# Performance work log

Hardware: AMD Instinct MI355X
Metric: run time of the kernel (lower is better)

## Reference

```python
import jax, jax.numpy as jnp
import numpy as np

NUM_ROUTES = 8 * 17 * 17  # 2312
NUM_CAPS = 10
OUT_CH = 16
IN_CH = 8


def squash(x, axis):
    sn = jnp.sum(x * x, axis=axis, keepdims=True)
    return sn * x / ((1.0 + sn) * jnp.sqrt(sn))


def setup_inputs() -> dict:
    key = jax.random.key(0)
    ks = jax.random.split(key, 11)
    B = 128
    data = jax.random.normal(ks[0], (B, 3, 49, 49), dtype=jnp.float32)
    conv_w = jax.random.normal(ks[1], (32, 3, 9, 9), dtype=jnp.float32) * 0.06
    conv_b = jax.random.normal(ks[2], (32,), dtype=jnp.float32) * 0.01
    # 8 primary-capsule convs, each 32->8, stacked: [8, 8, 32, 9, 9]
    prim_w = jax.random.normal(ks[3], (8, 8, 32, 9, 9), dtype=jnp.float32) * 0.02
    prim_b = jax.random.normal(ks[4], (8, 8), dtype=jnp.float32) * 0.01
    # DigitCaps W: torch used plain randn, shape [num_routes, num_caps, out, in]
    W_digit = jax.random.normal(ks[5], (NUM_ROUTES, NUM_CAPS, OUT_CH, IN_CH), dtype=jnp.float32)
    head_w1 = jax.random.normal(ks[6], (NUM_CAPS, 16, 100), dtype=jnp.float32) * 0.25
    head_b1 = jax.random.normal(ks[7], (NUM_CAPS, 100), dtype=jnp.float32) * 0.01
    head_w2 = jax.random.normal(ks[8], (NUM_CAPS, 100, 1), dtype=jnp.float32) * 0.1
    head_b2 = jax.random.normal(ks[9], (NUM_CAPS, 1), dtype=jnp.float32) * 0.01
    return {"data": data, "conv_w": conv_w, "conv_b": conv_b,
            "prim_w": prim_w, "prim_b": prim_b, "W_digit": W_digit,
            "head_w1": head_w1, "head_b1": head_b1,
            "head_w2": head_w2, "head_b2": head_b2}


def _forward(data, conv_w, conv_b, prim_w, prim_b, W_digit,
             head_w1, head_b1, head_w2, head_b2):
    dn = ("NCHW", "OIHW", "NCHW")
    # Conv stem: [B,3,49,49] -> [B,32,41,41], ReLU
    x = jax.lax.conv_general_dilated(data, conv_w, (1, 1), "VALID",
                                     dimension_numbers=dn)
    x = jax.nn.relu(x + conv_b[None, :, None, None])
    B = x.shape[0]
    # PrimaryCaps: 8 convs 32->8, k9 s2 -> [B,64,17,17] via merged weight
    pw = prim_w.reshape(64, 32, 9, 9)
    pb = prim_b.reshape(64)
    u = jax.lax.conv_general_dilated(x, pw, (2, 2), "VALID",
                                     dimension_numbers=dn)
    u = u + pb[None, :, None, None]
    u = u.reshape(B, 8, NUM_ROUTES)          # [B, 8 capsules, 2312]
    u = squash(u, axis=2)
    # DigitCaps: x_t [B, routes, in=8]; u_hat [B, routes, caps, out=16]
    x_t = u.transpose(0, 2, 1)
    u_hat = jnp.einsum("rcoi,bri->brco", W_digit, x_t)
    b_ij = jnp.zeros((NUM_ROUTES, NUM_CAPS), dtype=u_hat.dtype)
    v = None
    for it in range(3):
        c = jax.nn.softmax(b_ij, axis=1)                       # over capsules
        s = jnp.einsum("rc,brco->bco", c, u_hat)               # [B,caps,out]
        v = squash(s, axis=-1)                                 # [B,caps,16]
        if it < 2:
            a = jnp.einsum("brco,bco->brc", u_hat, v).mean(axis=0)
            b_ij = b_ij + a
    output = v[:, :, :, None]                                  # [B,10,16,1]
    # 10 tiny heads: head k applied to capsule k
    h = jnp.tanh(jnp.einsum("bci,cih->bch", v, head_w1) + head_b1[None])
    logits = jnp.einsum("bch,cho->bco", h, head_w2) + head_b2[None]
    cls = jax.nn.sigmoid(logits)                                # [B,10,1]
    return (output,) + tuple(cls[:, k] for k in range(NUM_CAPS))


def reference(data, conv_w, conv_b, prim_w, prim_b, W_digit,
              head_w1, head_b1, head_w2, head_b2):
    return _forward(data, conv_w, conv_b, prim_w, prim_b, W_digit,
                    head_w1, head_b1, head_w2, head_b2)
```

## Files before the change

kernel.cpp:

```cpp
#include <hip/hip_runtime.h>
#include <math.h>

#define BATCH 128
#define NR 2312
#define RC 34
#define NCH 68
#define NC 10
#define K1 352

typedef short short8 __attribute__((ext_vector_type(8)));
typedef float f32x4 __attribute__((ext_vector_type(4)));
typedef unsigned long long u64;

#define OFF_XH    0
#define OFF_XTB   3442688
#define OFF_SC    4630528
#define OFF_BIJ   4631552
#define OFF_SP    4654672
#define OFF_V     6047312
#define OFF_WB    6067792
#define OFF_VT    6150736
#define OFF_W1    6171216

__device__ __forceinline__ unsigned short f2bf(float f) {
    unsigned int u = __float_as_uint(f);
    u = (u + 0x7FFFu + ((u >> 16) & 1u)) >> 16;
    return (unsigned short)u;
}
__device__ __forceinline__ float bf2f(unsigned short h) {
    return __uint_as_float(((unsigned int)h) << 16);
}

__global__ void k_prep(const float* __restrict__ cw, const float* __restrict__ pw,
                       unsigned short* __restrict__ W1, unsigned short* __restrict__ Wb,
                       float* __restrict__ bij, float* __restrict__ scale) {
    int idx = blockIdx.x * 256 + threadIdx.x;
    if (idx < 165888) {
        int ci = idx & 31, co = (idx >> 5) & 15, cog = (idx >> 9) & 3, tap = idx >> 11;
        Wb[idx] = f2bf(pw[((cog * 16 + co) * 32 + ci) * 81 + tap]);
        return;
    }
    idx -= 165888;
    if (idx < 23120) { bij[idx] = 0.f; return; }
    idx -= 23120;
    if (idx < 1024) { scale[idx] = 0.f; return; }
    idx -= 1024;
    if (idx < 32 * K1) {
        int co = idx / K1, k = idx - co * K1;
        int g = k / 12, kw = k - g * 12;
        float v = (kw < 9 && g < 27) ? cw[((co * 3 + g / 9) * 9 + (g % 9)) * 9 + kw] : 0.f;
        W1[idx] = f2bf(v);
    }
}

__global__ __launch_bounds__(512) void k_conv1m(const float* __restrict__ data,
                                                const unsigned short* __restrict__ W1,
                                                const float* __restrict__ cb,
                                                unsigned short* __restrict__ xh) {
    int b = blockIdx.x / 27, g64 = blockIdx.x % 27;
    int p0 = g64 * 64;
    int t = threadIdx.x, lane = t & 63, wv = t >> 6;
    int quad = lane >> 4, mloc = lane & 15;
    int msub = wv & 3, chh = wv >> 2;
    __shared__ __align__(16) unsigned short As[88 * 64 * 4];
    u64* ab = (u64*)As;
    for (int k = 81 * 64 + t; k < 88 * 64; k += 512) ab[k] = 0ull;
#pragma unroll 1
    for (int it = 0; it < 4; it++) {
        int g = wv + it * 8;
        if (g < 27) {
            int m = lane;
            int p = p0 + m; if (p > 1680) p = 1680;
            int h = p / 41, w = p - h * 41;
            int ci = g / 9, kh = g - ci * 9;
            const float* src = &data[((b * 3 + ci) * 49 + (h + kh)) * 49 + w];
            unsigned short pk[12];
#pragma unroll
            for (int kw = 0; kw < 9; kw++) pk[kw] = f2bf(src[kw]);
            pk[9] = 0; pk[10] = 0; pk[11] = 0;
            const u64* s = (const u64*)pk;
            ab[(3 * g + 0) * 64 + m] = s[0];
            ab[(3 * g + 1) * 64 + m] = s[1];
            ab[(3 * g + 2) * 64 + m] = s[2];
        }
    }
    __syncthreads();
    f32x4 acc = {0.f, 0.f, 0.f, 0.f};
    const unsigned short* wp = &W1[(size_t)(chh * 16 + mloc) * K1 + quad * 8];
    int mrow = msub * 16 + mloc;
#pragma unroll 1
    for (int kc = 0; kc < 11; kc++) {
        int c = kc * 8 + quad * 2;
        union { short8 v; u64 q[2]; } af;
        af.q[0] = ab[c * 64 + mrow];
        af.q[1] = ab[(c + 1) * 64 + mrow];
        short8 bfr = *(const short8*)(wp + kc * 32);
        acc = __builtin_amdgcn_mfma_f32_16x16x32_bf16(af.v, bfr, acc, 0, 0, 0);
    }
    __syncthreads();
    unsigned short* tile = As;
    float bias = cb[chh * 16 + mloc];
#pragma unroll
    for (int r = 0; r < 4; r++) {
        int m = msub * 16 + quad * 4 + r;
        float v0 = acc[r] + bias; v0 = v0 > 0.f ? v0 : 0.f;
        tile[m * 40 + chh * 16 + mloc] = f2bf(v0);
    }
    __syncthreads();
    if (t < 256) {
        int m = t >> 2, part = t & 3;
        int p = p0 + m;
        if (p < 1681)
            *(int4*)&xh[((size_t)(b * 1681 + p)) * 32 + part * 8] =
                *(const int4*)&tile[m * 40 + part * 8];
    }
}

__global__ __launch_bounds__(512) void k_conv2(const unsigned short* __restrict__ xh,
                                               const unsigned short* __restrict__ Wb,
                                               const float* __restrict__ pb,
                                               unsigned short* __restrict__ xTb,
                                               float* __restrict__ scale) {
    const int pstart[5] = {0, 73, 145, 217, 289};
    int b = blockIdx.x >> 2, g = blockIdx.x & 3;
    int p0 = pstart[g], np = pstart[g + 1] - p0;
    int r0 = 2 * (p0 / 17);
    int t = threadIdx.x, lane = t & 63, wv = t >> 6;
    int quad = lane >> 4, mloc = lane & 15;
    int cg = wv & 3, th = wv >> 2;
    __shared__ __align__(16) char lds[50184];
    __shared__ float pbs[64];
    unsigned short* As = (unsigned short*)lds;
    if (t < 64) pbs[t] = pb[t];
    const unsigned short* xb = xh + (size_t)b * 53792;
    for (int k = t; k < 17 * 164; k += 512) {
        int rl = k / 164, rem = k - rl * 164;
        int col = rem >> 2, ci8 = rem & 3;
        int e = (col & 1) ? 21 + (col >> 1) : (col >> 1);
        const u64* src = (const u64*)&xb[((r0 + rl) * 41 + col) * 32 + ci8 * 8];
        u64* dst = (u64*)&As[(rl * 41 + e) * 36 + ci8 * 8];
        dst[0] = src[0];
        dst[1] = src[1];
    }
    __syncthreads();
    int abase[5];
#pragma unroll
    for (int mt = 0; mt < 5; mt++) {
        int p = p0 + mt * 16 + mloc;
        if (p > 288) p = 288;
        abase[mt] = ((2 * (p / 17) - r0) * 41 + (p % 17)) * 36 + quad * 8;
    }
    const unsigned short* wbase = Wb + ((size_t)cg * 16 + mloc) * 32 + quad * 8;
    f32x4 acc[5];
#pragma unroll
    for (int mt = 0; mt < 5; mt++)
#pragma unroll
        for (int r = 0; r < 4; r++) acc[mt][r] = 0.f;
    int kh0 = th ? 5 : 0, kh1 = th ? 9 : 5;
#pragma unroll 1
    for (int kh = kh0; kh < kh1; kh++) {
        const unsigned short* wrow = wbase + (size_t)kh * 9 * 2048;
#pragma unroll
        for (int kw = 0; kw < 9; kw++) {
            short8 bf = *(const short8*)(wrow + (size_t)kw * 2048);
            int c0 = (kw & 1) ? 21 + (kw >> 1) : (kw >> 1);
            int off = (kh * 41 + c0) * 36;
#pragma unroll
            for (int mt = 0; mt < 5; mt++) {
                union { short8 v; u64 q[2]; } a;
                a.q[0] = *(const u64*)&As[abase[mt] + off];
                a.q[1] = *(const u64*)&As[abase[mt] + off + 4];
                acc[mt] = __builtin_amdgcn_mfma_f32_16x16x32_bf16(a.v, bf, acc[mt], 0, 0, 0);
            }
        }
    }
    __syncthreads();
    float* tile = (float*)lds;
    if (th == 0) {
#pragma unroll
        for (int mt = 0; mt < 5; mt++)
#pragma unroll
            for (int r = 0; r < 4; r++)
                tile[(cg * 16 + mloc) * 81 + mt * 16 + quad * 4 + r] = acc[mt][r];
    }
    __syncthreads();
    if (th == 1) {
#pragma unroll
        for (int mt = 0; mt < 5; mt++)
#pragma unroll
            for (int r = 0; r < 4; r++)
                tile[(cg * 16 + mloc) * 81 + mt * 16 + quad * 4 + r] += acc[mt][r];
    }
    __syncthreads();
    float ssq[8] = {0.f, 0.f, 0.f, 0.f, 0.f, 0.f, 0.f, 0.f};
#pragma unroll 1
    for (int idx = t; idx < 8 * np; idx += 512) {
        int pp = idx >> 3, j = idx & 7;
        unsigned short pk[8];
#pragma unroll
        for (int i = 0; i < 8; i++) {
            float val = tile[(i * 8 + j) * 81 + pp] + pbs[i * 8 + j];
            pk[i] = f2bf(val);
            ssq[i] += val * val;
        }
        *(int4*)&xTb[((size_t)(j * 289 + p0 + pp) * 128 + b) * 8] = *(const int4*)pk;
    }
#pragma unroll
    for (int i = 0; i < 8; i++) {
        float s = ssq[i];
#pragma unroll
        for (int d = 1; d < 64; d <<= 1) s += __shfl_xor(s, d);
        if (lane == 0) atomicAdd(&scale[b * 8 + i], s);
    }
}

__global__ __launch_bounds__(256) void k_xt(unsigned short* __restrict__ xTb,
                                            const float* __restrict__ scale) {
    __shared__ float fs[1024];
    int t = threadIdx.x;
    for (int k = t; k < 1024; k += 256) {
        float sn = scale[k];
        fs[k] = sn / ((1.f + sn) * sqrtf(sn));
    }
    __syncthreads();
    int idx = blockIdx.x * 256 + t;
    int b = idx & 127;
    unsigned short* p = &xTb[(size_t)idx * 8];
    union { int4 v; unsigned short u[8]; } d;
    d.v = *(const int4*)p;
#pragma unroll
    for (int i = 0; i < 8; i++) d.u[i] = f2bf(bf2f(d.u[i]) * fs[b * 8 + i]);
    *(int4*)p = d.v;
}

__global__ __launch_bounds__(256) void k_s(const unsigned short* __restrict__ xTb,
                                           const float* __restrict__ W,
                                           const float* __restrict__ bij,
                                           float* __restrict__ spart) {
    int chunk = blockIdx.x / NC, c = blockIdx.x % NC;
    int r0 = chunk * RC;
    __shared__ __align__(16) unsigned short As[16 * 296];
    __shared__ float cs[RC];
    int t = threadIdx.x;
    { int o = t >> 4, kk = t & 15; As[o * 296 + 272 + kk] = 0; }
    if (t < RC) {
        int r = r0 + t;
        float x[NC], m = -1e30f;
#pragma unroll
        for (int k = 0; k < NC; k++) { x[k] = bij[r * NC + k]; m = fmaxf(m, x[k]); }
        float s = 0.f;
#pragma unroll
        for (int k = 0; k < NC; k++) { x[k] = expf(x[k] - m); s += x[k]; }
        cs[t] = x[c] / s;
    }
    __syncthreads();
    for (int k = t; k < RC * 16; k += 256) {
        int rr = k >> 4, o = k & 15;
        const float* wsrc = &W[(size_t)(r0 + rr) * 1280 + c * 128 + o * 8];
        float cr = cs[rr];
        unsigned short pk[8];
#pragma unroll
        for (int i = 0; i < 8; i++) pk[i] = f2bf(wsrc[i] * cr);
        *(int4*)&As[o * 296 + rr * 8] = *(const int4*)pk;
    }
    __syncthreads();
    int lane = t & 63, wv = t >> 6;
    int quad = lane >> 4, mloc = lane & 15;
    int n0 = wv * 32;
    f32x4 acc0 = {0.f, 0.f, 0.f, 0.f}, acc1 = {0.f, 0.f, 0.f, 0.f};
    const unsigned short* ap = &As[mloc * 296 + quad * 8];
#pragma unroll
    for (int kc = 0; kc < 9; kc++) {
        short8 af = *(const short8*)(ap + kc * 32);
        const unsigned short* bb = &xTb[(size_t)(r0 + kc * 4 + quad) * 1024];
        short8 b0 = *(const short8*)(bb + (n0 + mloc) * 8);
        short8 b1 = *(const short8*)(bb + (n0 + 16 + mloc) * 8);
        acc0 = __builtin_amdgcn_mfma_f32_16x16x32_bf16(af, b0, acc0, 0, 0, 0);
        acc1 = __builtin_amdgcn_mfma_f32_16x16x32_bf16(af, b1, acc1, 0, 0, 0);
    }
    float* sp = &spart[(size_t)(chunk * NC + c) * 2048];
    *(f32x4*)&sp[(n0 + mloc) * 16 + quad * 4] = acc0;
    *(f32x4*)&sp[(n0 + 16 + mloc) * 16 + quad * 4] = acc1;
}

__global__ __launch_bounds__(256) void k_v(const float* __restrict__ spart,
                    float* __restrict__ v, float* __restrict__ vT,
                    float* __restrict__ out,
                    const float* __restrict__ w1, const float* __restrict__ b1,
                    const float* __restrict__ w2, const float* __restrict__ b2,
                    int do_head) {
    int b = blockIdx.x / NC, c = blockIdx.x % NC;
    int t = threadIdx.x;
    int cl = t >> 4, o = t & 15;
    float s = 0.f;
#pragma unroll 1
    for (int ch = cl; ch < NCH; ch += 16)
        s += spart[((size_t)(ch * NC + c) * 128 + b) * 16 + o];
    s += __shfl_xor(s, 16);
    s += __shfl_xor(s, 32);
    __shared__ float red[4][16];
    __shared__ float hred[2];
    if ((t & 63) < 16) red[t >> 6][t & 15] = s;
    __syncthreads();
    if (t < 16) {
        float sum = red[0][t] + red[1][t] + red[2][t] + red[3][t];
        float sq = sum * sum;
#pragma unroll
        for (int d = 1; d < 16; d <<= 1) sq += __shfl_xor(sq, d);
        float vv = sum * sq / ((1.f + sq) * sqrtf(sq));
        int idx = (b * NC + c) * 16 + t;
        v[idx] = vv;
        out[idx] = vv;
        vT[(c * 16 + t) * 128 + b] = vv;
        red[0][t] = vv;
    }
    if (do_head) {
        __syncthreads();
        float partial = 0.f;
        if (t < 100) {
            float hs = b1[c * 100 + t];
#pragma unroll
            for (int i = 0; i < 16; i++) hs = fmaf(red[0][i], w1[(c * 16 + i) * 100 + t], hs);
            partial = tanhf(hs) * w2[c * 100 + t];
        }
#pragma unroll
        for (int d = 1; d < 64; d <<= 1) partial += __shfl_xor(partial, d);
        if ((t & 63) == 0 && t < 128) hred[t >> 6] = partial;
        __syncthreads();
        if (t == 0)
            out[20480 + c * 128 + b] = 1.f / (1.f + expf(-(hred[0] + hred[1] + b2[c])));
    }
}

__global__ __launch_bounds__(256) void k_a(const unsigned short* __restrict__ xTb,
                                           const float* __restrict__ W,
                                           const float* __restrict__ vT,
                                           float* __restrict__ bij) {
    int wv = threadIdx.x >> 6, lane = threadIdx.x & 63;
    int wid = __builtin_amdgcn_readfirstlane(blockIdx.x * 4 + wv);
    int r = wid / NC, c = wid - r * NC;
    const unsigned short* xr = &xTb[(size_t)r * 1024];
    union { short8 v; unsigned short u[8]; } s0, s1;
    s0.v = *(const short8*)(xr + lane * 8);
    s1.v = *(const short8*)(xr + (lane + 64) * 8);
    float x0[8], x1[8];
#pragma unroll
    for (int i = 0; i < 8; i++) { x0[i] = bf2f(s0.u[i]); x1[i] = bf2f(s1.u[i]); }
    const float* wr = &W[(size_t)r * 1280 + c * 128];
    const float* vc = &vT[c * 2048];
    float acc = 0.f;
#pragma unroll
    for (int o = 0; o < 16; o++) {
        float w[8];
#pragma unroll
        for (int i = 0; i < 8; i++) w[i] = wr[o * 8 + i];
        float u0 = 0.f, u1 = 0.f;
#pragma unroll
        for (int i = 0; i < 8; i++) { u0 = fmaf(w[i], x0[i], u0); u1 = fmaf(w[i], x1[i], u1); }
        acc = fmaf(vc[o * 128 + lane], u0, acc);
        acc = fmaf(vc[o * 128 + lane + 64], u1, acc);
    }
#pragma unroll
    for (int d = 1; d < 64; d <<= 1) acc += __shfl_xor(acc, d);
    if (lane == 0) bij[wid] += acc * 0.0078125f;
}

extern "C" void kernel_launch(void* const* d_in, const int* in_sizes, int n_in,
                              void* d_out, int out_size, void* d_ws, size_t ws_size,
                              hipStream_t stream) {
    const float* data   = (const float*)d_in[0];
    const float* conv_w = (const float*)d_in[1];
    const float* conv_b = (const float*)d_in[2];
    const float* prim_w = (const float*)d_in[3];
    const float* prim_b = (const float*)d_in[4];
    const float* Wd     = (const float*)d_in[5];
    const float* hw1    = (const float*)d_in[6];
    const float* hb1    = (const float*)d_in[7];
    const float* hw2    = (const float*)d_in[8];
    const float* hb2    = (const float*)d_in[9];
    float* ws = (float*)d_ws;
    unsigned short* xh  = (unsigned short*)(ws + OFF_XH);
    unsigned short* xTb = (unsigned short*)(ws + OFF_XTB);
    float* scale = ws + OFF_SC;
    float* bij   = ws + OFF_BIJ;
    float* spart = ws + OFF_SP;
    float* v     = ws + OFF_V;
    unsigned short* Wb  = (unsigned short*)(ws + OFF_WB);
    float* vT    = ws + OFF_VT;
    unsigned short* W1  = (unsigned short*)(ws + OFF_W1);
    float* out = (float*)d_out;

    k_prep<<<787, 256, 0, stream>>>(conv_w, prim_w, W1, Wb, bij, scale);
    k_conv1m<<<128 * 27, 512, 0, stream>>>(data, W1, conv_b, xh);
    k_conv2<<<128 * 4, 512, 0, stream>>>(xh, Wb, prim_b, xTb, scale);
    k_xt<<<1156, 256, 0, stream>>>(xTb, scale);
    for (int it = 0; it < 3; it++) {
        k_s<<<NCH * NC, 256, 0, stream>>>(xTb, Wd, bij, spart);
        k_v<<<128 * NC, 256, 0, stream>>>(spart, v, vT, out, hw1, hb1, hw2, hb2,
                                          it == 2 ? 1 : 0);
        if (it < 2) k_a<<<5780, 256, 0, stream>>>(xTb, Wd, vT, bij);
    }
}
```

Baseline: 234.0 us.

## Repartition primary-caps conv into 64-position tiles with M-split warps instead of K-split

The conv2 kernel now splits each image into 5 blocks of 64 output positions instead of 4 uneven groups. The two warp halves now take different M tiles (32 positions each, 2 accumulators) over the full 9x9 kernel, rather than splitting kh and summing partial results. This removes the two-pass reduction through shared memory and the extra MFMA tiles that were wasted on padding. It raises the grid to 640 blocks so more CUs get work, at the cost of more redundant halo loads of input rows per block.

```diff
diff --git a/kernel.cpp b/kernel.cpp
--- a/kernel.cpp
+++ b/kernel.cpp
@@ -121,19 +121,20 @@
                                                const float* __restrict__ pb,
                                                unsigned short* __restrict__ xTb,
                                                float* __restrict__ scale) {
-    const int pstart[5] = {0, 73, 145, 217, 289};
-    int b = blockIdx.x >> 2, g = blockIdx.x & 3;
-    int p0 = pstart[g], np = pstart[g + 1] - p0;
-    int r0 = 2 * (p0 / 17);
+    int b = blockIdx.x / 5, g = blockIdx.x % 5;
     int t = threadIdx.x, lane = t & 63, wv = t >> 6;
     int quad = lane >> 4, mloc = lane & 15;
-    int cg = wv & 3, th = wv >> 2;
+    int cg = wv & 3, half = wv >> 2;
     __shared__ __align__(16) char lds[50184];
     __shared__ float pbs[64];
     unsigned short* As = (unsigned short*)lds;
     if (t < 64) pbs[t] = pb[t];
     const unsigned short* xb = xh + (size_t)b * 53792;
-    for (int k = t; k < 17 * 164; k += 512) {
+    int p_hi = g * 64 + 63; if (p_hi > 288) p_hi = 288;
+    int r0 = 2 * ((g * 64) / 17);
+    int nrows = 2 * (p_hi / 17) + 9 - r0;
+    int nch = nrows * 164;
+    for (int k = t; k < nch; k += 512) {
         int rl = k / 164, rem = k - rl * 164;
         int col = rem >> 2, ci8 = rem & 3;
         int e = (col & 1) ? 21 + (col >> 1) : (col >> 1);
@@ -143,67 +144,56 @@
         dst[1] = src[1];
     }
     __syncthreads();
-    int abase[5];
-#pragma unroll
-    for (int mt = 0; mt < 5; mt++) {
-        int p = p0 + mt * 16 + mloc;
+    int abase0, abase1;
+    {
+        int p = g * 64 + half * 32 + mloc;
         if (p > 288) p = 288;
-        abase[mt] = ((2 * (p / 17) - r0) * 41 + (p % 17)) * 36 + quad * 8;
+        abase0 = ((2 * (p / 17) - r0) * 41 + (p % 17)) * 36 + quad * 8;
+        p = g * 64 + half * 32 + 16 + mloc;
+        if (p > 288) p = 288;
+        abase1 = ((2 * (p / 17) - r0) * 41 + (p % 17)) * 36 + quad * 8;
     }
     const unsigned short* wbase = Wb + ((size_t)cg * 16 + mloc) * 32 + quad * 8;
-    f32x4 acc[5];
-#pragma unroll
-    for (int mt = 0; mt < 5; mt++)
-#pragma unroll
-        for (int r = 0; r < 4; r++) acc[mt][r] = 0.f;
-    int kh0 = th ? 5 : 0, kh1 = th ? 9 : 5;
+    f32x4 acc0 = {0.f, 0.f, 0.f, 0.f}, acc1 = {0.f, 0.f, 0.f, 0.f};
 #pragma unroll 1
-    for (int kh = kh0; kh < kh1; kh++) {
+    for (int kh = 0; kh < 9; kh++) {
         const unsigned short* wrow = wbase + (size_t)kh * 9 * 2048;
 #pragma unroll
         for (int kw = 0; kw < 9; kw++) {
             short8 bf = *(const short8*)(wrow + (size_t)kw * 2048);
             int c0 = (kw & 1) ? 21 + (kw >> 1) : (kw >> 1);
             int off = (kh * 41 + c0) * 36;
-#pragma unroll
-            for (int mt = 0; mt < 5; mt++) {
-                union { short8 v; u64 q[2]; } a;
-                a.q[0] = *(const u64*)&As[abase[mt] + off];
-                a.q[1] = *(const u64*)&As[abase[mt] + off + 4];
-                acc[mt] = __builtin_amdgcn_mfma_f32_16x16x32_bf16(a.v, bf, acc[mt], 0, 0, 0);
+            union { short8 v; u64 q[2]; } a0, a1;
+            a0.q[0] = *(const u64*)&As[abase0 + off];
+            a0.q[1] = *(const u64*)&As[abase0 + off + 4];
+            a1.q[0] = *(const u64*)&As[abase1 + off];
+            a1.q[1] = *(const u64*)&As[abase1 + off + 4];
+            acc0 = __builtin_amdgcn_mfma_f32_16x16x32_bf16(a0.v, bf, acc0, 0, 0, 0);
+            acc1 = __builtin_amdgcn_mfma_f32_16x16x32_bf16(a1.v, bf, acc1, 0, 0, 0);
+        }
+    }
+    __syncthreads();
+    float* tile = (float*)lds;
+#pragma unroll
+    for (int r = 0; r < 4; r++) {
+        tile[(cg * 16 + mloc) * 65 + half * 32 + quad * 4 + r] = acc0[r];
+        tile[(cg * 16 + mloc) * 65 + half * 32 + 16 + quad * 4 + r] = acc1[r];
+    }
+    __syncthreads();
+    float ssq[8] = {0.f, 0.f, 0.f, 0.f, 0.f, 0.f, 0.f, 0.f};
+    {
+        int pp = t >> 3, j = t & 7;
+        int p = g * 64 + pp;
+        if (p < 289) {
+            unsigned short pk[8];
+#pragma unroll
+            for (int i = 0; i < 8; i++) {
+                float val = tile[(i * 8 + j) * 65 + pp] + pbs[i * 8 + j];
+                pk[i] = f2bf(val);
+                ssq[i] += val * val;
             }
+            *(int4*)&xTb[((size_t)(j * 289 + p) * 128 + b) * 8] = *(const int4*)pk;
         }
-    }
-    __syncthreads();
-    float* tile = (float*)lds;
-    if (th == 0) {
-#pragma unroll
-        for (int mt = 0; mt < 5; mt++)
-#pragma unroll
-            for (int r = 0; r < 4; r++)
-                tile[(cg * 16 + mloc) * 81 + mt * 16 + quad * 4 + r] = acc[mt][r];
-    }
-    __syncthreads();
-    if (th == 1) {
-#pragma unroll
-        for (int mt = 0; mt < 5; mt++)
-#pragma unroll
-            for (int r = 0; r < 4; r++)
-                tile[(cg * 16 + mloc) * 81 + mt * 16 + quad * 4 + r] += acc[mt][r];
-    }
-    __syncthreads();
-    float ssq[8] = {0.f, 0.f, 0.f, 0.f, 0.f, 0.f, 0.f, 0.f};
-#pragma unroll 1
-    for (int idx = t; idx < 8 * np; idx += 512) {
-        int pp = idx >> 3, j = idx & 7;
-        unsigned short pk[8];
-#pragma unroll
-        for (int i = 0; i < 8; i++) {
-            float val = tile[(i * 8 + j) * 81 + pp] + pbs[i * 8 + j];
-            pk[i] = f2bf(val);
-            ssq[i] += val * val;
-        }
-        *(int4*)&xTb[((size_t)(j * 289 + p0 + pp) * 128 + b) * 8] = *(const int4*)pk;
     }
 #pragma unroll
     for (int i = 0; i < 8; i++) {
@@ -392,7 +382,7 @@
 
     k_prep<<<787, 256, 0, stream>>>(conv_w, prim_w, W1, Wb, bij, scale);
     k_conv1m<<<128 * 27, 512, 0, stream>>>(data, W1, conv_b, xh);
-    k_conv2<<<128 * 4, 512, 0, stream>>>(xh, Wb, prim_b, xTb, scale);
+    k_conv2<<<128 * 5, 512, 0, stream>>>(xh, Wb, prim_b, xTb, scale);
     k_xt<<<1156, 256, 0, stream>>>(xTb, scale);
     for (int it = 0; it < 3; it++) {
         k_s<<<NCH * NC, 256, 0, stream>>>(xTb, Wd, bij, spart);
```

Result: slower. 244.3 us (+4.4%).
